# Kernel optimization log

Hardware: AMD Instinct MI355X
Metric: run time of the kernel (lower is better)

## Reference

```python
import jax, jax.numpy as jnp
import numpy as np

B, N, D = 4, 2048, 512
H, DH = 8, 64  # heads, dim_head; inner_dim = H*DH = 512
SCALE = DH ** -0.5


def setup_inputs() -> dict:
    key = jax.random.key(0)
    kx, kw = jax.random.split(key)
    x = jax.random.normal(kx, (B, N, D), dtype=jnp.float32)
    # torch Linear weight layout: [out_features=3*H*DH, in_features=D]
    W_qkv = jax.random.normal(kw, (3 * H * DH, D), dtype=jnp.float32) * 0.02
    return {"x": x, "W_qkv": W_qkv}


def reference(x, W_qkv):
    b, n, d = x.shape
    # qkv projection (no bias since qkv_bias=False)
    qkv = x @ W_qkv.T                                  # [b, n, 3*H*DH]
    qkv = qkv.reshape(b, n, 3, H, DH).transpose(2, 0, 3, 1, 4)  # [3, b, H, n, DH]
    q, k, v = qkv[0], qkv[1], qkv[2]
    # shifted query: q_cross[t] = q[t-1] for t>=1, q_cross[0] = q[0]
    q_cross = jnp.concatenate([q[:, :, :1, :], q[:, :, :-1, :]], axis=2)
    scores = jnp.einsum("bhqd,bhkd->bhqk", q_cross * SCALE, k)  # [b, H, n, n]
    attn = jax.nn.softmax(scores, axis=-1)
    out = jnp.einsum("bhqk,bhkd->bhqd", attn, v)       # [b, H, n, DH]
    out = out.transpose(0, 2, 1, 3).reshape(b, n, H * DH)
    # to_out is Dropout(0.0) -> identity in eval / p=0
    return out
```

## Files before the change

kernel.cpp:

```cpp
#include <hip/hip_runtime.h>
#include <hip/hip_bf16.h>
#include <stdint.h>

typedef __bf16 bf16_t;
typedef float floatx4 __attribute__((ext_vector_type(4)));
typedef __bf16 bf16x8 __attribute__((ext_vector_type(8)));
typedef __bf16 bf16x4 __attribute__((ext_vector_type(4)));

#define QSCALE 0.1803368801111204f

__device__ __forceinline__ void gl2lds16(const bf16_t* g, bf16_t* l) {
    __builtin_amdgcn_global_load_lds(
        (const __attribute__((address_space(1))) unsigned int*)g,
        (__attribute__((address_space(3))) unsigned int*)l,
        16, 0, 0);
}

__global__ __launch_bounds__(256) void convert_kernel(const float* __restrict__ x,
                                                      bf16_t* __restrict__ xb,
                                                      const float* __restrict__ w,
                                                      bf16_t* __restrict__ wb,
                                                      int nx4) {
    int i = blockIdx.x * 256 + threadIdx.x;
    const float* in; bf16_t* out; int j;
    if (i < nx4) { in = x; out = xb; j = i; }
    else         { in = w; out = wb; j = i - nx4; }
    float4 v = ((const float4*)in)[j];
    bf16x4 o;
    o.x = (bf16_t)v.x; o.y = (bf16_t)v.y; o.z = (bf16_t)v.z; o.w = (bf16_t)v.w;
    ((bf16x4*)out)[j] = o;
}

__global__ __launch_bounds__(256) void qkv_gemm(const bf16_t* __restrict__ X,
                                                const bf16_t* __restrict__ W,
                                                bf16_t* __restrict__ Q,
                                                bf16_t* __restrict__ K,
                                                bf16_t* __restrict__ Vt)
{
    __shared__ bf16_t As[128 * 64];
    __shared__ bf16_t Bs[128 * 64];

    const int tid  = threadIdx.x;
    const int wave = tid >> 6;
    const int lane = tid & 63;
    const int quad = lane >> 4;
    const int lrow = lane & 15;
    const int t7g  = lrow & 7;
    const int bm0 = blockIdx.x * 128;
    const int bn0 = blockIdx.y * 128;
    const int mw = (wave >> 1) * 64;
    const int nw = (wave & 1) * 64;
    const int wbase = tid & 192;

    floatx4 acc[4][4];
#pragma unroll
    for (int i = 0; i < 4; i++)
#pragma unroll
        for (int j = 0; j < 4; j++) acc[i][j] = (floatx4)0.0f;

#pragma unroll 1
    for (int kb = 0; kb < 8; ++kb) {
        const int k0 = kb * 64;
        __syncthreads();
#pragma unroll
        for (int r = 0; r < 4; ++r) {
            int c = r * 256 + tid;
            int row = c >> 3, kc = c & 7;
            int skc = kc ^ (row & 7);
            gl2lds16(X + (size_t)(bm0 + row) * 512 + k0 + skc * 8,
                     As + (size_t)(r * 256 + wbase) * 8);
        }
#pragma unroll
        for (int r = 0; r < 4; ++r) {
            int c = r * 256 + tid;
            int row = c >> 3, kc = c & 7;
            int skc = kc ^ (row & 7);
            gl2lds16(W + (size_t)(bn0 + row) * 512 + k0 + skc * 8,
                     Bs + (size_t)(r * 256 + wbase) * 8);
        }
        __syncthreads();
#pragma unroll
        for (int ks = 0; ks < 2; ++ks) {
            bf16x8 af[4], bfr[4];
#pragma unroll
            for (int mi = 0; mi < 4; mi++)
                af[mi] = *(const bf16x8*)(As + (mw + mi * 16 + lrow) * 64 + (((ks * 4 + quad) ^ t7g) << 3));
#pragma unroll
            for (int ni = 0; ni < 4; ni++)
                bfr[ni] = *(const bf16x8*)(Bs + (nw + ni * 16 + lrow) * 64 + (((ks * 4 + quad) ^ t7g) << 3));
#pragma unroll
            for (int mi = 0; mi < 4; mi++)
#pragma unroll
                for (int ni = 0; ni < 4; ni++)
                    acc[mi][ni] = __builtin_amdgcn_mfma_f32_16x16x32_bf16(af[mi], bfr[ni], acc[mi][ni], 0, 0, 0);
        }
    }

#pragma unroll
    for (int mi = 0; mi < 4; mi++) {
        int mbase = bm0 + mw + mi * 16 + quad * 4;
        int b = mbase >> 11, n = mbase & 2047;
#pragma unroll
        for (int ni = 0; ni < 4; ni++) {
            int o = bn0 + nw + ni * 16 + lrow;
            int s  = o >> 9;
            int h  = (o >> 6) & 7;
            int dh = o & 63;
            int bh = b * 8 + h;
            if (s == 2) {
                bf16x4 pv;
#pragma unroll
                for (int r = 0; r < 4; r++) pv[r] = (bf16_t)acc[mi][ni][r];
                *(bf16x4*)(Vt + ((size_t)bh * 64 + dh) * 2048 + n) = pv;
            } else if (s == 0) {
#pragma unroll
                for (int r = 0; r < 4; r++)
                    Q[((size_t)bh * 2048 + n + r) * 64 + dh] = (bf16_t)(acc[mi][ni][r] * QSCALE);
            } else {
#pragma unroll
                for (int r = 0; r < 4; r++)
                    K[((size_t)bh * 2048 + n + r) * 64 + dh] = (bf16_t)acc[mi][ni][r];
            }
        }
    }
}

__device__ __forceinline__ void stage_tile(const bf16_t* __restrict__ kb,
                                           const bf16_t* __restrict__ vb,
                                           int kt, bf16_t* ksbuf, bf16_t* vsbuf,
                                           int wave, int lane) {
#pragma unroll
    for (int part = 0; part < 2; ++part) {
        int ch  = part * 256 + wave * 64 + lane;
        int row = ch >> 3, cc = ch & 7;
        int scc = cc ^ (row & 7);
        bf16_t* ldst = ksbuf + (size_t)(part * 256 + wave * 64) * 8;
        gl2lds16(kb + ((size_t)(kt * 64 + row)) * 64 + scc * 8, ldst);
        bf16_t* ldst2 = vsbuf + (size_t)(part * 256 + wave * 64) * 8;
        gl2lds16(vb + (size_t)row * 2048 + kt * 64 + scc * 8, ldst2);
    }
}

__global__ __launch_bounds__(256) void flash_attn(const bf16_t* __restrict__ Q,
                                                  const bf16_t* __restrict__ K,
                                                  const bf16_t* __restrict__ Vt,
                                                  float* __restrict__ Out)
{
    __shared__ bf16_t Ks[2][64 * 64];
    __shared__ bf16_t Vs[2][64 * 64];
    __shared__ bf16_t Ps[4][16 * 64];

    const int tid  = threadIdx.x;
    const int wave = tid >> 6;
    const int lane = tid & 63;
    const int quad = lane >> 4;
    const int c    = lane & 15;
    const int t7   = c & 7;
    const int qt = blockIdx.x;
    const int bh = blockIdx.y;
    const int b = bh >> 3, h = bh & 7;

    int qg  = qt * 64 + wave * 16 + c;
    int src = (qg == 0) ? 0 : qg - 1;
    const bf16_t* qbase = Q + ((size_t)bh * 2048 + src) * 64;
    bf16x8 qf0 = *(const bf16x8*)(qbase + quad * 8);
    bf16x8 qf1 = *(const bf16x8*)(qbase + 32 + quad * 8);

    floatx4 o[4];
#pragma unroll
    for (int i = 0; i < 4; i++) o[i] = (floatx4)0.0f;
    float lacc[4] = {0.f, 0.f, 0.f, 0.f};

    const bf16_t* kb = K + ((size_t)bh * 2048) * 64;
    const bf16_t* vb = Vt + ((size_t)bh * 64) * 2048;
    bf16_t* pw = Ps[wave];

    stage_tile(kb, vb, 0, Ks[0], Vs[0], wave, lane);

#pragma unroll 1
    for (int kt = 0; kt < 32; ++kt) {
        const int buf = kt & 1;
        __syncthreads();
        if (kt < 31)
            stage_tile(kb, vb, kt + 1, Ks[buf ^ 1], Vs[buf ^ 1], wave, lane);

        const bf16_t* ks = Ks[buf];
        const bf16_t* vs = Vs[buf];

        floatx4 s[4];
#pragma unroll
        for (int sub = 0; sub < 4; ++sub) {
            const bf16_t* krow = ks + (sub * 16 + c) * 64;
            bf16x8 kf0 = *(const bf16x8*)(krow + ((quad ^ t7) << 3));
            bf16x8 kf1 = *(const bf16x8*)(krow + (((4 + quad) ^ t7) << 3));
            floatx4 t = (floatx4)0.0f;
            t = __builtin_amdgcn_mfma_f32_16x16x32_bf16(qf0, kf0, t, 0, 0, 0);
            t = __builtin_amdgcn_mfma_f32_16x16x32_bf16(qf1, kf1, t, 0, 0, 0);
            s[sub] = t;
        }

#pragma unroll
        for (int sub = 0; sub < 4; ++sub)
#pragma unroll
            for (int r = 0; r < 4; r++) {
                float p = __builtin_amdgcn_exp2f(s[sub][r]);
                lacc[r] += p;
                int row  = quad * 4 + r;
                int col8 = sub * 2 + (c >> 3);
                pw[row * 64 + ((col8 ^ (row & 7)) << 3) + t7] = (bf16_t)p;
            }

#pragma unroll
        for (int ki = 0; ki < 2; ++ki) {
            bf16x8 pf = *(const bf16x8*)(pw + c * 64 + (((ki * 4 + quad) ^ t7) << 3));
#pragma unroll
            for (int sub = 0; sub < 4; ++sub) {
                const bf16_t* vrow = vs + (sub * 16 + c) * 64;
                bf16x8 vf = *(const bf16x8*)(vrow + (((ki * 4 + quad) ^ t7) << 3));
                o[sub] = __builtin_amdgcn_mfma_f32_16x16x32_bf16(pf, vf, o[sub], 0, 0, 0);
            }
        }
    }

#pragma unroll
    for (int r = 0; r < 4; r++)
#pragma unroll
        for (int d = 1; d < 16; d <<= 1)
            lacc[r] += __shfl_xor(lacc[r], d, 64);

    int n0 = qt * 64 + wave * 16 + quad * 4;
    float* ob = Out + (size_t)b * 2048 * 512 + (size_t)h * 64;
#pragma unroll
    for (int r = 0; r < 4; r++) {
        float inv = 1.0f / lacc[r];
        float* orow = ob + (size_t)(n0 + r) * 512;
#pragma unroll
        for (int sub = 0; sub < 4; ++sub)
            orow[sub * 16 + c] = o[sub][r] * inv;
    }
}

extern "C" void kernel_launch(void* const* d_in, const int* in_sizes, int n_in,
                              void* d_out, int out_size, void* d_ws, size_t ws_size,
                              hipStream_t stream) {
    const float* x = (const float*)d_in[0];
    const float* w = (const float*)d_in[1];
    float* out = (float*)d_out;

    char* ws = (char*)d_ws;
    bf16_t* xb = (bf16_t*)(ws);
    bf16_t* wb = (bf16_t*)(ws + 8388608);
    bf16_t* q  = (bf16_t*)(ws + 9961472);
    bf16_t* k  = (bf16_t*)(ws + 18350080);
    bf16_t* vt = (bf16_t*)(ws + 26738688);

    convert_kernel<<<4864, 256, 0, stream>>>(x, xb, w, wb, 1048576);
    qkv_gemm<<<dim3(64, 12), 256, 0, stream>>>(xb, wb, q, k, vt);
    flash_attn<<<dim3(32, 32), 256, 0, stream>>>(q, k, vt, out);
}
```

Measured before the change: 154.4 us.

## Split key tile across wave pairs with 32-row query tiles and LDS reduction

Each pair of waves now owns 32 query rows and each wave of the pair handles half of every 64-key tile. K and V fragments loaded from LDS are reused across two query subtiles. The partial outputs and row sums are merged through LDS at the end. This halves LDS fragment reads per MFMA but adds a final exchange with extra syncs and doubles accumulator registers.

```diff
diff --git a/kernel.cpp b/kernel.cpp
--- a/kernel.cpp
+++ b/kernel.cpp
@@ -156,20 +156,28 @@
     const int quad = lane >> 4;
     const int c    = lane & 15;
     const int t7   = c & 7;
+    const int p = wave >> 1;
+    const int e = wave & 1;
     const int qt = blockIdx.x;
     const int bh = blockIdx.y;
     const int b = bh >> 3, h = bh & 7;
 
-    int qg  = qt * 64 + wave * 16 + c;
-    int src = (qg == 0) ? 0 : qg - 1;
-    const bf16_t* qbase = Q + ((size_t)bh * 2048 + src) * 64;
-    bf16x8 qf0 = *(const bf16x8*)(qbase + quad * 8);
-    bf16x8 qf1 = *(const bf16x8*)(qbase + 32 + quad * 8);
-
-    floatx4 o[4];
-#pragma unroll
-    for (int i = 0; i < 4; i++) o[i] = (floatx4)0.0f;
-    float lacc[4] = {0.f, 0.f, 0.f, 0.f};
+    bf16x8 qf[2][2];
+#pragma unroll
+    for (int qsub = 0; qsub < 2; qsub++) {
+        int qg  = qt * 64 + p * 32 + qsub * 16 + c;
+        int src = (qg == 0) ? 0 : qg - 1;
+        const bf16_t* qb = Q + ((size_t)bh * 2048 + src) * 64;
+        qf[qsub][0] = *(const bf16x8*)(qb + quad * 8);
+        qf[qsub][1] = *(const bf16x8*)(qb + 32 + quad * 8);
+    }
+
+    floatx4 o[2][4];
+#pragma unroll
+    for (int qsub = 0; qsub < 2; qsub++)
+#pragma unroll
+        for (int i = 0; i < 4; i++) o[qsub][i] = (floatx4)0.0f;
+    float lacc[2][4] = {{0.f,0.f,0.f,0.f},{0.f,0.f,0.f,0.f}};
 
     const bf16_t* kb = K + ((size_t)bh * 2048) * 64;
     const bf16_t* vb = Vt + ((size_t)bh * 64) * 2048;
@@ -187,56 +195,83 @@
         const bf16_t* ks = Ks[buf];
         const bf16_t* vs = Vs[buf];
 
-        floatx4 s[4];
-#pragma unroll
-        for (int sub = 0; sub < 4; ++sub) {
-            const bf16_t* krow = ks + (sub * 16 + c) * 64;
+        floatx4 s[2][2];
+#pragma unroll
+        for (int ksub = 0; ksub < 2; ++ksub) {
+            const bf16_t* krow = ks + (e * 32 + ksub * 16 + c) * 64;
             bf16x8 kf0 = *(const bf16x8*)(krow + ((quad ^ t7) << 3));
             bf16x8 kf1 = *(const bf16x8*)(krow + (((4 + quad) ^ t7) << 3));
-            floatx4 t = (floatx4)0.0f;
-            t = __builtin_amdgcn_mfma_f32_16x16x32_bf16(qf0, kf0, t, 0, 0, 0);
-            t = __builtin_amdgcn_mfma_f32_16x16x32_bf16(qf1, kf1, t, 0, 0, 0);
-            s[sub] = t;
-        }
-
-#pragma unroll
-        for (int sub = 0; sub < 4; ++sub)
-#pragma unroll
-            for (int r = 0; r < 4; r++) {
-                float p = __builtin_amdgcn_exp2f(s[sub][r]);
-                lacc[r] += p;
-                int row  = quad * 4 + r;
-                int col8 = sub * 2 + (c >> 3);
-                pw[row * 64 + ((col8 ^ (row & 7)) << 3) + t7] = (bf16_t)p;
+#pragma unroll
+            for (int qsub = 0; qsub < 2; ++qsub) {
+                floatx4 t = (floatx4)0.0f;
+                t = __builtin_amdgcn_mfma_f32_16x16x32_bf16(qf[qsub][0], kf0, t, 0, 0, 0);
+                t = __builtin_amdgcn_mfma_f32_16x16x32_bf16(qf[qsub][1], kf1, t, 0, 0, 0);
+                s[qsub][ksub] = t;
             }
-
-#pragma unroll
-        for (int ki = 0; ki < 2; ++ki) {
-            bf16x8 pf = *(const bf16x8*)(pw + c * 64 + (((ki * 4 + quad) ^ t7) << 3));
-#pragma unroll
-            for (int sub = 0; sub < 4; ++sub) {
-                const bf16_t* vrow = vs + (sub * 16 + c) * 64;
-                bf16x8 vf = *(const bf16x8*)(vrow + (((ki * 4 + quad) ^ t7) << 3));
-                o[sub] = __builtin_amdgcn_mfma_f32_16x16x32_bf16(pf, vf, o[sub], 0, 0, 0);
-            }
-        }
-    }
-
+        }
+
+#pragma unroll
+        for (int qsub = 0; qsub < 2; ++qsub)
+#pragma unroll
+            for (int ksub = 0; ksub < 2; ++ksub)
+#pragma unroll
+                for (int r = 0; r < 4; r++) {
+                    float pv = __builtin_amdgcn_exp2f(s[qsub][ksub][r]);
+                    lacc[qsub][r] += pv;
+                    int row = quad * 4 + r;
+                    int chl = qsub * 4 + ksub * 2 + (c >> 3);
+                    pw[row * 64 + ((chl ^ (row & 7)) << 3) + t7] = (bf16_t)pv;
+                }
+
+        bf16x8 pf[2];
+#pragma unroll
+        for (int qsub = 0; qsub < 2; ++qsub)
+            pf[qsub] = *(const bf16x8*)(pw + c * 64 + (((qsub * 4 + quad) ^ t7) << 3));
+#pragma unroll
+        for (int dsub = 0; dsub < 4; ++dsub) {
+            const bf16_t* vrow = vs + (dsub * 16 + c) * 64;
+            bf16x8 vf = *(const bf16x8*)(vrow + (((e * 4 + quad) ^ t7) << 3));
+#pragma unroll
+            for (int qsub = 0; qsub < 2; ++qsub)
+                o[qsub][dsub] = __builtin_amdgcn_mfma_f32_16x16x32_bf16(pf[qsub], vf, o[qsub][dsub], 0, 0, 0);
+        }
+    }
+
+#pragma unroll
+    for (int qsub = 0; qsub < 2; ++qsub)
+#pragma unroll
+        for (int r = 0; r < 4; r++)
+#pragma unroll
+            for (int d = 1; d < 16; d <<= 1)
+                lacc[qsub][r] += __shfl_xor(lacc[qsub][r], d, 64);
+
+    __syncthreads();
+    float* oex = (float*)&Ks[0][0];
+    float* lex = (float*)&Vs[0][0];
+    const int pe = e ^ 1;
+#pragma unroll
+    for (int dsub = 0; dsub < 4; ++dsub)
+#pragma unroll
+        for (int r = 0; r < 4; r++)
+            oex[wave * 1024 + (quad * 4 + r) * 64 + dsub * 16 + c] = o[pe][dsub][r];
 #pragma unroll
     for (int r = 0; r < 4; r++)
-#pragma unroll
-        for (int d = 1; d < 16; d <<= 1)
-            lacc[r] += __shfl_xor(lacc[r], d, 64);
-
-    int n0 = qt * 64 + wave * 16 + quad * 4;
+        lex[wave * 16 + quad * 4 + r] = lacc[pe][r];
+    __syncthreads();
+
+    const int pwav = wave ^ 1;
+    int n0 = qt * 64 + p * 32 + e * 16 + quad * 4;
     float* ob = Out + (size_t)b * 2048 * 512 + (size_t)h * 64;
 #pragma unroll
     for (int r = 0; r < 4; r++) {
-        float inv = 1.0f / lacc[r];
+        float lsum = lacc[e][r] + lex[pwav * 16 + quad * 4 + r];
+        float inv = 1.0f / lsum;
         float* orow = ob + (size_t)(n0 + r) * 512;
 #pragma unroll
-        for (int sub = 0; sub < 4; ++sub)
-            orow[sub * 16 + c] = o[sub][r] * inv;
+        for (int dsub = 0; dsub < 4; ++dsub) {
+            float val = o[e][dsub][r] + oex[pwav * 1024 + (quad * 4 + r) * 64 + dsub * 16 + c];
+            orow[dsub * 16 + c] = val * inv;
+        }
     }
 }
 
```

Result: slower. 177.8 us (+15.2%).

## Switch flash attention to 32x32x16 MFMA with 128-query tiles per block

Applied to the files above, without the earlier changes.

Each wave now owns 32 query rows instead of 16 and uses the 32x32x16 bf16 MFMA for both the QK^T and PV products, so a block covers 128 queries and the grid halves. Each K/V tile staged into shared memory is reused across twice as many queries, and each MFMA does more work per issue. The cost is more accumulator and row-sum registers per thread (16 sums, two 16-wide outputs), a larger per-wave P buffer in shared memory, and only 512 blocks, which may reduce occupancy and CU utilisation.

```diff
diff --git a/kernel.cpp b/kernel.cpp
--- a/kernel.cpp
+++ b/kernel.cpp
@@ -4,6 +4,7 @@
 
 typedef __bf16 bf16_t;
 typedef float floatx4 __attribute__((ext_vector_type(4)));
+typedef float floatx16 __attribute__((ext_vector_type(16)));
 typedef __bf16 bf16x8 __attribute__((ext_vector_type(8)));
 typedef __bf16 bf16x4 __attribute__((ext_vector_type(4)));
 
@@ -148,28 +149,30 @@
 {
     __shared__ bf16_t Ks[2][64 * 64];
     __shared__ bf16_t Vs[2][64 * 64];
-    __shared__ bf16_t Ps[4][16 * 64];
+    __shared__ bf16_t Ps[4][32 * 64];
 
     const int tid  = threadIdx.x;
     const int wave = tid >> 6;
     const int lane = tid & 63;
-    const int quad = lane >> 4;
-    const int c    = lane & 15;
-    const int t7   = c & 7;
+    const int m    = lane & 31;
+    const int e5   = lane >> 5;
     const int qt = blockIdx.x;
     const int bh = blockIdx.y;
     const int b = bh >> 3, h = bh & 7;
 
-    int qg  = qt * 64 + wave * 16 + c;
+    int qg  = qt * 128 + wave * 32 + m;
     int src = (qg == 0) ? 0 : qg - 1;
-    const bf16_t* qbase = Q + ((size_t)bh * 2048 + src) * 64;
-    bf16x8 qf0 = *(const bf16x8*)(qbase + quad * 8);
-    bf16x8 qf1 = *(const bf16x8*)(qbase + 32 + quad * 8);
-
-    floatx4 o[4];
-#pragma unroll
-    for (int i = 0; i < 4; i++) o[i] = (floatx4)0.0f;
-    float lacc[4] = {0.f, 0.f, 0.f, 0.f};
+    const bf16_t* qb = Q + ((size_t)bh * 2048 + src) * 64;
+    bf16x8 qf[4];
+#pragma unroll
+    for (int dc = 0; dc < 4; ++dc)
+        qf[dc] = *(const bf16x8*)(qb + dc * 16 + e5 * 8);
+
+    floatx16 o[2];
+    o[0] = (floatx16)0.0f; o[1] = (floatx16)0.0f;
+    float lacc[16];
+#pragma unroll
+    for (int r = 0; r < 16; r++) lacc[r] = 0.0f;
 
     const bf16_t* kb = K + ((size_t)bh * 2048) * 64;
     const bf16_t* vb = Vt + ((size_t)bh * 64) * 2048;
@@ -187,56 +190,53 @@
         const bf16_t* ks = Ks[buf];
         const bf16_t* vs = Vs[buf];
 
-        floatx4 s[4];
-#pragma unroll
-        for (int sub = 0; sub < 4; ++sub) {
-            const bf16_t* krow = ks + (sub * 16 + c) * 64;
-            bf16x8 kf0 = *(const bf16x8*)(krow + ((quad ^ t7) << 3));
-            bf16x8 kf1 = *(const bf16x8*)(krow + (((4 + quad) ^ t7) << 3));
-            floatx4 t = (floatx4)0.0f;
-            t = __builtin_amdgcn_mfma_f32_16x16x32_bf16(qf0, kf0, t, 0, 0, 0);
-            t = __builtin_amdgcn_mfma_f32_16x16x32_bf16(qf1, kf1, t, 0, 0, 0);
-            s[sub] = t;
-        }
-
-#pragma unroll
-        for (int sub = 0; sub < 4; ++sub)
-#pragma unroll
-            for (int r = 0; r < 4; r++) {
-                float p = __builtin_amdgcn_exp2f(s[sub][r]);
-                lacc[r] += p;
-                int row  = quad * 4 + r;
-                int col8 = sub * 2 + (c >> 3);
-                pw[row * 64 + ((col8 ^ (row & 7)) << 3) + t7] = (bf16_t)p;
-            }
-
-#pragma unroll
-        for (int ki = 0; ki < 2; ++ki) {
-            bf16x8 pf = *(const bf16x8*)(pw + c * 64 + (((ki * 4 + quad) ^ t7) << 3));
-#pragma unroll
-            for (int sub = 0; sub < 4; ++sub) {
-                const bf16_t* vrow = vs + (sub * 16 + c) * 64;
-                bf16x8 vf = *(const bf16x8*)(vrow + (((ki * 4 + quad) ^ t7) << 3));
-                o[sub] = __builtin_amdgcn_mfma_f32_16x16x32_bf16(pf, vf, o[sub], 0, 0, 0);
-            }
-        }
-    }
-
-#pragma unroll
-    for (int r = 0; r < 4; r++)
-#pragma unroll
-        for (int d = 1; d < 16; d <<= 1)
-            lacc[r] += __shfl_xor(lacc[r], d, 64);
-
-    int n0 = qt * 64 + wave * 16 + quad * 4;
+#pragma unroll
+        for (int kt2 = 0; kt2 < 2; ++kt2) {
+            const int key = kt2 * 32 + m;
+            const bf16_t* krow = ks + key * 64;
+            const int kx = key & 7;
+            floatx16 s = (floatx16)0.0f;
+#pragma unroll
+            for (int dc = 0; dc < 4; ++dc) {
+                bf16x8 kf = *(const bf16x8*)(krow + (((dc * 2 + e5) ^ kx) << 3));
+                s = __builtin_amdgcn_mfma_f32_32x32x16_bf16(qf[dc], kf, s, 0, 0, 0);
+            }
+#pragma unroll
+            for (int reg = 0; reg < 16; ++reg) {
+                float p = __builtin_amdgcn_exp2f(s[reg]);
+                lacc[reg] += p;
+                int row = (reg & 3) + 8 * (reg >> 2) + 4 * e5;
+                int c8  = kt2 * 4 + (m >> 3);
+                pw[row * 64 + ((c8 ^ (row & 7)) << 3) + (m & 7)] = (bf16_t)p;
+            }
+        }
+
+#pragma unroll
+        for (int kc = 0; kc < 4; ++kc) {
+            bf16x8 pf = *(const bf16x8*)(pw + m * 64 + (((kc * 2 + e5) ^ (m & 7)) << 3));
+#pragma unroll
+            for (int dt = 0; dt < 2; ++dt) {
+                const int drow = dt * 32 + m;
+                bf16x8 vf = *(const bf16x8*)(vs + drow * 64 + (((kc * 2 + e5) ^ (drow & 7)) << 3));
+                o[dt] = __builtin_amdgcn_mfma_f32_32x32x16_bf16(pf, vf, o[dt], 0, 0, 0);
+            }
+        }
+    }
+
+#pragma unroll
+    for (int reg = 0; reg < 16; ++reg)
+#pragma unroll
+        for (int d = 1; d < 32; d <<= 1)
+            lacc[reg] += __shfl_xor(lacc[reg], d, 64);
+
     float* ob = Out + (size_t)b * 2048 * 512 + (size_t)h * 64;
 #pragma unroll
-    for (int r = 0; r < 4; r++) {
-        float inv = 1.0f / lacc[r];
-        float* orow = ob + (size_t)(n0 + r) * 512;
-#pragma unroll
-        for (int sub = 0; sub < 4; ++sub)
-            orow[sub * 16 + c] = o[sub][r] * inv;
+    for (int reg = 0; reg < 16; ++reg) {
+        int qrow = qt * 128 + wave * 32 + (reg & 3) + 8 * (reg >> 2) + 4 * e5;
+        float inv = 1.0f / lacc[reg];
+        float* orow = ob + (size_t)qrow * 512;
+        orow[m]      = o[0][reg] * inv;
+        orow[32 + m] = o[1][reg] * inv;
     }
 }
 
@@ -256,5 +256,5 @@
 
     convert_kernel<<<4864, 256, 0, stream>>>(x, xb, w, wb, 1048576);
     qkv_gemm<<<dim3(64, 12), 256, 0, stream>>>(xb, wb, q, k, vt);
-    flash_attn<<<dim3(32, 32), 256, 0, stream>>>(q, k, vt, out);
-}
+    flash_attn<<<dim3(16, 32), 256, 0, stream>>>(q, k, vt, out);
+}
```

New measurement: 155.6 us. No clear change (+0.8%).
